# Performance work log

Measured on AMD Instinct MI355X. Metric: run time of the kernel, lower is better.

Reference implementation:

```python
import jax, jax.numpy as jnp
import numpy as np

DIM = 192
D_STATE = 16
D_CONV = 4
EXPAND = 2
D_INNER = EXPAND * DIM
DT_RANK = -(-DIM // 16)  # ceil(dim/16) = 12


def setup_inputs() -> dict:
    key = jax.random.key(0)
    ks = jax.random.split(key, 9)
    B, T, H, W, C = 2, 16, 28, 28, DIM
    x = jax.random.normal(ks[0], (B, T, H, W, C), dtype=jnp.float32)
    s = lambda k, shp, fan: jax.random.normal(k, shp, dtype=jnp.float32) / np.sqrt(fan)
    params = {
        "norm_w": jnp.ones((DIM,), jnp.float32),
        "in_proj_w": s(ks[1], (DIM, 2 * D_INNER), DIM),
        "conv_w": s(ks[2], (D_INNER, D_CONV), D_CONV),
        "conv_b": jnp.zeros((D_INNER,), jnp.float32),
        "x_proj_w": s(ks[3], (D_INNER, DT_RANK + 2 * D_STATE), D_INNER),
        "dt_proj_w": s(ks[4], (DT_RANK, D_INNER), DT_RANK),
        "dt_proj_b": jnp.full((D_INNER,), float(np.log(np.expm1(0.01))), jnp.float32),
        "A_log": jnp.log(jnp.broadcast_to(jnp.arange(1, D_STATE + 1, dtype=jnp.float32), (D_INNER, D_STATE))),
        "D": jnp.ones((D_INNER,), jnp.float32),
        "out_proj_w": s(ks[5], (D_INNER, DIM), D_INNER),
    }
    return {"x": x, **params}


def _mamba_block(xs, norm_w, in_proj_w, conv_w, conv_b, x_proj_w,
                 dt_proj_w, dt_proj_b, A_log, D, out_proj_w):
    # xs: (N, T, C). Pre-RMSNorm + Mamba + residual.
    nrm = jax.lax.rsqrt(jnp.mean(xs * xs, axis=-1, keepdims=True) + 1e-6)
    xn = xs * nrm * norm_w

    xz = xn @ in_proj_w                      # (N, T, 2*Din)
    u, z = jnp.split(xz, 2, axis=-1)         # each (N, T, Din)

    # causal depthwise conv over T
    uc = jnp.transpose(u, (0, 2, 1))         # (N, Din, T)
    uc = jax.lax.conv_general_dilated(
        uc, conv_w[:, None, :], window_strides=(1,),
        padding=[(D_CONV - 1, 0)], feature_group_count=D_INNER)
    uc = jax.nn.silu(uc + conv_b[None, :, None])
    uc = jnp.transpose(uc, (0, 2, 1))        # (N, T, Din)

    dbl = uc @ x_proj_w                      # (N, T, dt_rank + 2*S)
    dt, Bm, Cm = jnp.split(dbl, [DT_RANK, DT_RANK + D_STATE], axis=-1)
    dt = jax.nn.softplus(dt @ dt_proj_w + dt_proj_b)   # (N, T, Din)
    A = -jnp.exp(A_log)                      # (Din, S)

    def step(h, inp):
        dt_t, B_t, C_t, u_t = inp            # (N,Din),(N,S),(N,S),(N,Din)
        dA = jnp.exp(dt_t[..., None] * A)    # (N, Din, S)
        h = h * dA + (dt_t * u_t)[..., None] * B_t[:, None, :]
        y = jnp.einsum('nds,ns->nd', h, C_t)
        return h, y

    N = uc.shape[0]
    h0 = jnp.zeros((N, D_INNER, D_STATE), dt.dtype)
    sw = lambda a: jnp.swapaxes(a, 0, 1)     # time-major for scan
    _, ys = jax.lax.scan(step, h0, (sw(dt), sw(Bm), sw(Cm), sw(uc)))
    y = jnp.swapaxes(ys, 0, 1) + uc * D      # (N, T, Din)
    y = y * jax.nn.silu(z)
    return xs + y @ out_proj_w


def reference(x, norm_w, in_proj_w, conv_w, conv_b, x_proj_w,
              dt_proj_w, dt_proj_b, A_log, D, out_proj_w):
    B, T, H, W, C = x.shape
    xs = jnp.transpose(x, (0, 2, 3, 1, 4)).reshape(B * H * W, T, C)
    out = _mamba_block(xs, norm_w, in_proj_w, conv_w, conv_b, x_proj_w,
                       dt_proj_w, dt_proj_b, A_log, D, out_proj_w)
    return jnp.transpose(out.reshape(B, H, W, T, C), (0, 3, 1, 2, 4))
```

## Files before the change

### kernel.cpp

```cpp
#include <hip/hip_runtime.h>

#define NSEQ 1568
#define TDIM 16
#define CDIM 192
#define DIN  384
#define SDIM 16
#define RNK  12
#define XZW  768
#define DBLW 44
#define HW784 784

#define XNP  200
#define DINP 392
#define DBLP 48

#define NT_IN 48
#define KT_IN 6
#define NT_OUT 12
#define KT_OUT 12
#define NT_XP 3
#define KT_XP 12
#define GRP_IN  (NT_IN*KT_IN*64)
#define GRP_OUT (NT_OUT*KT_OUT*64)
#define GRP_XP  (NT_XP*KT_XP*64)
#define OFF_OUT (GRP_IN*8)
#define OFF_XP  (OFF_OUT + GRP_OUT*8)
#define WS_NEED ((size_t)(OFF_XP + GRP_XP*8) * 2)

#define IN_EL  (CDIM*XZW)
#define OUT_EL (DIN*CDIM)
#define XP_EL  (GRP_XP*8)
#define PACK_TOT (IN_EL + OUT_EL + XP_EL)

typedef unsigned short u16;
typedef unsigned int   u32;
typedef __attribute__((ext_vector_type(8))) short short8;
typedef __attribute__((ext_vector_type(4))) float f32x4;

#define LOG2E 1.44269504f
#define LN2   0.69314718f

__device__ __forceinline__ float bf2f(u16 u) {
  union { u32 i; float f; } c; c.i = ((u32)u) << 16; return c.f;
}
__device__ __forceinline__ u16 f2bf(float f) {
  union { float f; u32 i; } c; c.f = f;
  u32 i = c.i;
  i += 0x7FFFu + ((i >> 16) & 1u);
  return (u16)(i >> 16);
}

__device__ __forceinline__ float ex2(float x) {
#if __has_builtin(__builtin_amdgcn_exp2f)
  return __builtin_amdgcn_exp2f(x);
#else
  return exp2f(x);
#endif
}
__device__ __forceinline__ float lg2(float x) {
#if __has_builtin(__builtin_amdgcn_logf)
  return __builtin_amdgcn_logf(x);
#else
  return log2f(x);
#endif
}
__device__ __forceinline__ float frcp(float x) {
#if __has_builtin(__builtin_amdgcn_rcpf)
  return __builtin_amdgcn_rcpf(x);
#else
  return 1.0f / x;
#endif
}
__device__ __forceinline__ float sigmoid_f(float s) {
  return frcp(1.0f + ex2(-LOG2E * s));
}
__device__ __forceinline__ float softplus_f(float a) {
  return fmaxf(a, 0.f) + LN2 * lg2(1.0f + ex2(-LOG2E * fabsf(a)));
}

template<bool B16>
__device__ __forceinline__ float ldg(const void* p, int i) {
  if (B16) return bf2f(((const u16*)p)[i]);
  return ((const float*)p)[i];
}
template<bool B16>
__device__ __forceinline__ void stg(void* p, int i, float v) {
  if (B16) ((u16*)p)[i] = f2bf(v);
  else     ((float*)p)[i] = v;
}

__device__ __forceinline__ bool probe_bf16(const void* x) {
  const u16* xu = (const u16*)x;
  int plaus = 0;
  #pragma unroll
  for (int k = 0; k < 32; ++k) {
    u16 v = xu[2*k];
    int e = (v >> 7) & 0xFF;
    plaus += ((e >= 100 && e <= 140) || v == 0) ? 1 : 0;
  }
  return plaus >= 16;
}

template<bool B16>
__device__ __forceinline__ void pack_body(const void* in_w, const void* out_w,
                                          const void* xp_w, u16* ws, int e) {
  if (e < IN_EL) {
    int k = e / XZW, n = e - k*XZW;
    int nt = n >> 4, l16 = n & 15, kt = k >> 5, q8 = (k & 31) >> 3, j = k & 7;
    int lane = q8*16 + l16;
    ws[((nt*KT_IN + kt)*64 + lane)*8 + j] = f2bf(ldg<B16>(in_w, e));
  } else if (e < IN_EL + OUT_EL) {
    int ee = e - IN_EL;
    int k = ee / CDIM, n = ee - k*CDIM;
    int nt = n >> 4, l16 = n & 15, kt = k >> 5, q8 = (k & 31) >> 3, j = k & 7;
    int lane = q8*16 + l16;
    ws[OFF_OUT + ((nt*KT_OUT + kt)*64 + lane)*8 + j] = f2bf(ldg<B16>(out_w, ee));
  } else if (e < PACK_TOT) {
    int ee = e - IN_EL - OUT_EL;
    int gg = ee >> 3, j = ee & 7;
    int lane = gg & 63, kt = (gg >> 6) % KT_XP, nt = gg / (64*KT_XP);
    int k = kt*32 + (lane >> 4)*8 + j, n = nt*16 + (lane & 15);
    ws[OFF_XP + ee] = f2bf(n < DBLW ? ldg<B16>(xp_w, k*DBLW + n) : 0.f);
  }
}

__global__ void pack_w(const void* __restrict__ x, const void* __restrict__ in_w,
                       const void* __restrict__ out_w, const void* __restrict__ xp_w,
                       u16* __restrict__ ws) {
  int e = blockIdx.x * blockDim.x + threadIdx.x;
  if (probe_bf16(x)) pack_body<true >(in_w, out_w, xp_w, ws, e);
  else               pack_body<false>(in_w, out_w, xp_w, ws, e);
}

struct Smem {
  float dbl[TDIM*DBLP];
  u16   xn [TDIM*XNP];
  u16   u  [TDIM*DINP];
  u16   z  [TDIM*DINP];
};

template<bool B16>
__device__ __forceinline__ void body(
    Smem& sm, const u16* __restrict__ ws,
    const void* __restrict__ x,        const void* __restrict__ norm_w,
    const void* __restrict__ conv_w,   const void* __restrict__ conv_b,
    const void* __restrict__ dt_proj_w,const void* __restrict__ dt_proj_b,
    const void* __restrict__ A_log,    const void* __restrict__ Dp,
    void* __restrict__ out)
{
  const int tid  = threadIdx.x;
  const int wid  = tid >> 6;
  const int lane = tid & 63;
  const int quad = lane >> 4;
  const int l16  = lane & 15;
  const int n  = blockIdx.x;
  const int b  = n / HW784;
  const int hw = n - b * HW784;

  {
    const int c0 = lane, c1 = lane + 64, c2 = lane + 128;
    float nw0 = ldg<B16>(norm_w, c0), nw1 = ldg<B16>(norm_w, c1), nw2 = ldg<B16>(norm_w, c2);
    for (int t = wid; t < TDIM; t += 6) {
      int base = ((b*TDIM + t)*HW784 + hw)*CDIM;
      float v0 = ldg<B16>(x, base + c0);
      float v1 = ldg<B16>(x, base + c1);
      float v2 = ldg<B16>(x, base + c2);
      float ss = v0*v0 + v1*v1 + v2*v2;
      #pragma unroll
      for (int off = 32; off > 0; off >>= 1) ss += __shfl_xor(ss, off, 64);
      float rs = rsqrtf(ss * (1.0f/CDIM) + 1e-6f);
      sm.xn[t*XNP + c0] = f2bf(v0 * rs * nw0);
      sm.xn[t*XNP + c1] = f2bf(v1 * rs * nw1);
      sm.xn[t*XNP + c2] = f2bf(v2 * rs * nw2);
    }
  }
  __syncthreads();

  {
    short8 afr[KT_IN];
    #pragma unroll
    for (int kt = 0; kt < KT_IN; ++kt)
      afr[kt] = *(const short8*)(sm.xn + l16*XNP + kt*32 + quad*8);
    #pragma unroll
    for (int g = 0; g < 2; ++g) {
      f32x4 acc[4];
      #pragma unroll
      for (int i = 0; i < 4; ++i) acc[i] = (f32x4)0.f;
      #pragma unroll
      for (int kt = 0; kt < KT_IN; ++kt) {
        #pragma unroll
        for (int i = 0; i < 4; ++i) {
          int ntg = wid*8 + g*4 + i;
          short8 bfr = *(const short8*)(ws + ((ntg*KT_IN + kt)*64 + lane)*8);
          acc[i] = __builtin_amdgcn_mfma_f32_16x16x32_bf16(afr[kt], bfr, acc[i], 0, 0, 0);
        }
      }
      #pragma unroll
      for (int i = 0; i < 4; ++i) {
        int ntg = wid*8 + g*4 + i;
        u16* dst = (ntg < 24) ? sm.u : sm.z;
        int col = ((ntg < 24) ? ntg*16 : (ntg-24)*16) + l16;
        #pragma unroll
        for (int r = 0; r < 4; ++r)
          dst[(quad*4 + r)*DINP + col] = f2bf(acc[i][r]);
      }
    }
  }
  __syncthreads();

  {
    const int d = tid;
    float w0 = ldg<B16>(conv_w, d*4+0), w1 = ldg<B16>(conv_w, d*4+1);
    float w2 = ldg<B16>(conv_w, d*4+2), w3 = ldg<B16>(conv_w, d*4+3);
    float bias = ldg<B16>(conv_b, d);
    float um1 = 0.f, um2 = 0.f, um3 = 0.f;
    #pragma unroll
    for (int t = 0; t < TDIM; ++t) {
      float cur = bf2f(sm.u[t*DINP + d]);
      float s = bias + cur*w3 + um1*w2 + um2*w1 + um3*w0;
      um3 = um2; um2 = um1; um1 = cur;
      sm.u[t*DINP + d] = f2bf(s * sigmoid_f(s));
    }
  }

  float wd[RNK];
  float dt_bias = ldg<B16>(dt_proj_b, tid);
  #pragma unroll
  for (int r = 0; r < RNK; ++r) wd[r] = ldg<B16>(dt_proj_w, r*DIN + tid);
  float Dv = ldg<B16>(Dp, tid);
  float a2;
  bool geo;
  {
    a2 = -LOG2E * ex2(LOG2E * ldg<B16>(A_log, tid*SDIM + 0));
    geo = true;
    #pragma unroll
    for (int s = 1; s < SDIM; ++s) {
      float as = -LOG2E * ex2(LOG2E * ldg<B16>(A_log, tid*SDIM + s));
      geo = geo && (fabsf(as - (float)(s+1)*a2) <= 1e-4f * fabsf(as) + 1e-30f);
    }
  }
  __syncthreads();

  if (wid < 3) {
    f32x4 acc = (f32x4)0.f;
    #pragma unroll
    for (int kt = 0; kt < KT_XP; ++kt) {
      short8 afr = *(const short8*)(sm.u + l16*DINP + kt*32 + quad*8);
      short8 bfr = *(const short8*)(ws + OFF_XP + ((wid*KT_XP + kt)*64 + lane)*8);
      acc = __builtin_amdgcn_mfma_f32_16x16x32_bf16(afr, bfr, acc, 0, 0, 0);
    }
    #pragma unroll
    for (int r = 0; r < 4; ++r)
      sm.dbl[(quad*4 + r)*DBLP + wid*16 + l16] = acc[r];
  }
  __syncthreads();

  {
    const int d = tid;
    float h[SDIM];
    #pragma unroll
    for (int s = 0; s < SDIM; ++s) h[s] = 0.f;
    if (geo) {
      for (int t = 0; t < TDIM; ++t) {
        const float* row = sm.dbl + t*DBLP;
        f32x4 d0 = *(const f32x4*)(row + 0);
        f32x4 d1 = *(const f32x4*)(row + 4);
        f32x4 d2 = *(const f32x4*)(row + 8);
        float a = dt_bias
          + d0[0]*wd[0] + d0[1]*wd[1] + d0[2]*wd[2]  + d0[3]*wd[3]
          + d1[0]*wd[4] + d1[1]*wd[5] + d1[2]*wd[6]  + d1[3]*wd[7]
          + d2[0]*wd[8] + d2[1]*wd[9] + d2[2]*wd[10] + d2[3]*wd[11];
        float dtv = softplus_f(a);
        float uv  = bf2f(sm.u[t*DINP + d]);
        float du  = dtv * uv;
        float q = ex2(dtv * a2);
        float Pq[SDIM];
        Pq[0] = q;        Pq[1] = q*q;       Pq[2] = Pq[1]*q;     Pq[3] = Pq[1]*Pq[1];
        Pq[4] = Pq[3]*q;  Pq[5] = Pq[3]*Pq[1]; Pq[6] = Pq[3]*Pq[2]; Pq[7] = Pq[3]*Pq[3];
        Pq[8] = Pq[7]*q;  Pq[9] = Pq[7]*Pq[1]; Pq[10]= Pq[7]*Pq[2]; Pq[11]= Pq[7]*Pq[3];
        Pq[12]= Pq[7]*Pq[4]; Pq[13]= Pq[7]*Pq[5]; Pq[14]= Pq[7]*Pq[6]; Pq[15]= Pq[7]*Pq[7];
        float y = 0.f;
        #pragma unroll
        for (int g = 0; g < 4; ++g) {
          f32x4 Bv = *(const f32x4*)(row + 12 + 4*g);
          f32x4 Cv = *(const f32x4*)(row + 28 + 4*g);
          #pragma unroll
          for (int j = 0; j < 4; ++j) {
            int s = 4*g + j;
            h[s] = h[s]*Pq[s] + du*Bv[j];
            y += h[s]*Cv[j];
          }
        }
        y += uv * Dv;
        float zv = bf2f(sm.z[t*DINP + d]);
        sm.z[t*DINP + d] = f2bf(y * (zv * sigmoid_f(zv)));
      }
    } else {
      float A2[SDIM];
      #pragma unroll
      for (int s = 0; s < SDIM; ++s)
        A2[s] = -LOG2E * ex2(LOG2E * ldg<B16>(A_log, d*SDIM + s));
      for (int t = 0; t < TDIM; ++t) {
        const float* row = sm.dbl + t*DBLP;
        f32x4 d0 = *(const f32x4*)(row + 0);
        f32x4 d1 = *(const f32x4*)(row + 4);
        f32x4 d2 = *(const f32x4*)(row + 8);
        float a = dt_bias
          + d0[0]*wd[0] + d0[1]*wd[1] + d0[2]*wd[2]  + d0[3]*wd[3]
          + d1[0]*wd[4] + d1[1]*wd[5] + d1[2]*wd[6]  + d1[3]*wd[7]
          + d2[0]*wd[8] + d2[1]*wd[9] + d2[2]*wd[10] + d2[3]*wd[11];
        float dtv = softplus_f(a);
        float uv  = bf2f(sm.u[t*DINP + d]);
        float du  = dtv * uv;
        float y = 0.f;
        #pragma unroll
        for (int g = 0; g < 4; ++g) {
          f32x4 Bv = *(const f32x4*)(row + 12 + 4*g);
          f32x4 Cv = *(const f32x4*)(row + 28 + 4*g);
          #pragma unroll
          for (int j = 0; j < 4; ++j) {
            int s = 4*g + j;
            float dA = ex2(dtv * A2[s]);
            h[s] = h[s]*dA + du*Bv[j];
            y += h[s]*Cv[j];
          }
        }
        y += uv * Dv;
        float zv = bf2f(sm.z[t*DINP + d]);
        sm.z[t*DINP + d] = f2bf(y * (zv * sigmoid_f(zv)));
      }
    }
  }
  __syncthreads();

  {
    f32x4 acc[2];
    acc[0] = (f32x4)0.f; acc[1] = (f32x4)0.f;
    #pragma unroll
    for (int kt = 0; kt < KT_OUT; ++kt) {
      short8 afr = *(const short8*)(sm.z + l16*DINP + kt*32 + quad*8);
      #pragma unroll
      for (int i = 0; i < 2; ++i) {
        int ntg = wid*2 + i;
        short8 bfr = *(const short8*)(ws + OFF_OUT + ((ntg*KT_OUT + kt)*64 + lane)*8);
        acc[i] = __builtin_amdgcn_mfma_f32_16x16x32_bf16(afr, bfr, acc[i], 0, 0, 0);
      }
    }
    #pragma unroll
    for (int i = 0; i < 2; ++i) {
      int col = (wid*2 + i)*16 + l16;
      #pragma unroll
      for (int r = 0; r < 4; ++r) {
        int row = quad*4 + r;
        int gi = ((b*TDIM + row)*HW784 + hw)*CDIM + col;
        float o = ldg<B16>(x, gi) + acc[i][r];
        stg<B16>(out, gi, o);
      }
    }
  }
}

__launch_bounds__(384, 6)
__global__ void mamba_mfma(
    const u16* __restrict__ ws,
    const void* __restrict__ x,        const void* __restrict__ norm_w,
    const void* __restrict__ conv_w,   const void* __restrict__ conv_b,
    const void* __restrict__ dt_proj_w,const void* __restrict__ dt_proj_b,
    const void* __restrict__ A_log,    const void* __restrict__ Dp,
    void* __restrict__ out)
{
  __shared__ Smem sm;
  if (probe_bf16(x))
    body<true >(sm, ws, x, norm_w, conv_w, conv_b, dt_proj_w, dt_proj_b, A_log, Dp, out);
  else
    body<false>(sm, ws, x, norm_w, conv_w, conv_b, dt_proj_w, dt_proj_b, A_log, Dp, out);
}

struct SmemF {
  float dt [TDIM*DIN];
  float dbl[TDIM*DBLW];
  u16   xs [TDIM*CDIM];
  u16   xn [TDIM*CDIM];
  u16   u  [TDIM*DIN];
  u16   z  [TDIM*DIN];
};

template<bool B16>
__device__ __forceinline__ void body_fb(
    SmemF& sm,
    const void* __restrict__ x,        const void* __restrict__ norm_w,
    const void* __restrict__ in_proj_w,const void* __restrict__ conv_w,
    const void* __restrict__ conv_b,   const void* __restrict__ x_proj_w,
    const void* __restrict__ dt_proj_w,const void* __restrict__ dt_proj_b,
    const void* __restrict__ A_log,    const void* __restrict__ Dp,
    const void* __restrict__ out_proj_w, void* __restrict__ out)
{
  const int tid = threadIdx.x;
  const int n  = blockIdx.x;
  const int b  = n / HW784;
  const int hw = n - b * HW784;

  for (int i = tid; i < TDIM*CDIM; i += 384) {
    int t = i / CDIM, c = i - t * CDIM;
    sm.xs[i] = f2bf(ldg<B16>(x, ((b*TDIM + t)*HW784 + hw)*CDIM + c));
  }
  __syncthreads();
  {
    int wave = tid >> 6, lane = tid & 63;
    for (int t = wave; t < TDIM; t += 6) {
      float ss = 0.f;
      for (int c = lane; c < CDIM; c += 64) {
        float v = bf2f(sm.xs[t*CDIM + c]); ss += v*v;
      }
      #pragma unroll
      for (int off = 32; off > 0; off >>= 1) ss += __shfl_xor(ss, off, 64);
      float rs = rsqrtf(ss * (1.0f/CDIM) + 1e-6f);
      for (int c = lane; c < CDIM; c += 64)
        sm.xn[t*CDIM + c] = f2bf(bf2f(sm.xs[t*CDIM + c]) * rs * ldg<B16>(norm_w, c));
    }
  }
  __syncthreads();
  {
    float acc0[TDIM], acc1[TDIM];
    #pragma unroll
    for (int t = 0; t < TDIM; ++t) { acc0[t] = 0.f; acc1[t] = 0.f; }
    const int j0 = 2 * tid;
    for (int c = 0; c < CDIM; c += 2) {
      float wA0 = ldg<B16>(in_proj_w,  c   *XZW + j0);
      float wA1 = ldg<B16>(in_proj_w,  c   *XZW + j0 + 1);
      float wB0 = ldg<B16>(in_proj_w, (c+1)*XZW + j0);
      float wB1 = ldg<B16>(in_proj_w, (c+1)*XZW + j0 + 1);
      #pragma unroll
      for (int t = 0; t < TDIM; ++t) {
        union { u32 i; float f; } c0, c1;
        u32 xv = *(const u32*)(sm.xn + t*CDIM + c);
        c0.i = xv << 16; c1.i = xv & 0xFFFF0000u;
        acc0[t] += c0.f*wA0 + c1.f*wB0;
        acc1[t] += c0.f*wA1 + c1.f*wB1;
      }
    }
    if (tid < 192) {
      #pragma unroll
      for (int t = 0; t < TDIM; ++t) {
        sm.u[t*DIN + j0]   = f2bf(acc0[t]);
        sm.u[t*DIN + j0+1] = f2bf(acc1[t]);
      }
    } else {
      int z0 = j0 - 384;
      #pragma unroll
      for (int t = 0; t < TDIM; ++t) {
        sm.z[t*DIN + z0]   = f2bf(acc0[t]);
        sm.z[t*DIN + z0+1] = f2bf(acc1[t]);
      }
    }
  }
  __syncthreads();
  {
    const int d = tid;
    float uv[TDIM];
    #pragma unroll
    for (int t = 0; t < TDIM; ++t) uv[t] = bf2f(sm.u[t*DIN + d]);
    float w0 = ldg<B16>(conv_w, d*4+0), w1 = ldg<B16>(conv_w, d*4+1);
    float w2 = ldg<B16>(conv_w, d*4+2), w3 = ldg<B16>(conv_w, d*4+3);
    float bias = ldg<B16>(conv_b, d);
    #pragma unroll
    for (int t = 0; t < TDIM; ++t) {
      float s = bias + uv[t]*w3;
      if (t >= 1) s += uv[t-1]*w2;
      if (t >= 2) s += uv[t-2]*w1;
      if (t >= 3) s += uv[t-3]*w0;
      float sg = 1.0f / (1.0f + __expf(-s));
      sm.u[t*DIN + d] = f2bf(s * sg);
    }
  }
  __syncthreads();
  for (int o = tid; o < TDIM*DBLW; o += 384) {
    int t = o / DBLW, j = o - t*DBLW;
    float acc = 0.f;
    for (int d = 0; d < DIN; ++d)
      acc += bf2f(sm.u[t*DIN + d]) * ldg<B16>(x_proj_w, d*DBLW + j);
    sm.dbl[o] = acc;
  }
  __syncthreads();
  {
    const int d = tid;
    float wd[RNK];
    #pragma unroll
    for (int r = 0; r < RNK; ++r) wd[r] = ldg<B16>(dt_proj_w, r*DIN + d);
    float bias = ldg<B16>(dt_proj_b, d);
    #pragma unroll
    for (int t = 0; t < TDIM; ++t) {
      float a = bias;
      #pragma unroll
      for (int r = 0; r < RNK; ++r) a += sm.dbl[t*DBLW + r] * wd[r];
      sm.dt[t*DIN + d] = fmaxf(a, 0.f) + log1pf(__expf(-fabsf(a)));
    }
  }
  __syncthreads();
  {
    const int d = tid;
    float A[SDIM], h[SDIM];
    #pragma unroll
    for (int s = 0; s < SDIM; ++s) {
      A[s] = -__expf(ldg<B16>(A_log, d*SDIM + s));
      h[s] = 0.f;
    }
    float Dv = ldg<B16>(Dp, d);
    for (int t = 0; t < TDIM; ++t) {
      float dtv = sm.dt[t*DIN + d];
      float uv  = bf2f(sm.u[t*DIN + d]);
      float du  = dtv * uv;
      float y = 0.f;
      #pragma unroll
      for (int s = 0; s < SDIM; ++s) {
        float dA = __expf(dtv * A[s]);
        h[s] = h[s]*dA + du * sm.dbl[t*DBLW + 12 + s];
        y += h[s] * sm.dbl[t*DBLW + 28 + s];
      }
      y += uv * Dv;
      float zv = bf2f(sm.z[t*DIN + d]);
      float sg = 1.0f / (1.0f + __expf(-zv));
      sm.dt[t*DIN + d] = y * (zv * sg);
    }
  }
  __syncthreads();
  {
    const int tt = tid / CDIM;
    const int c  = tid - tt*CDIM;
    float acc[8];
    #pragma unroll
    for (int i = 0; i < 8; ++i) acc[i] = 0.f;
    for (int d = 0; d < DIN; ++d) {
      float w = ldg<B16>(out_proj_w, d*CDIM + c);
      #pragma unroll
      for (int i = 0; i < 8; ++i)
        acc[i] += sm.dt[(tt*8 + i)*DIN + d] * w;
    }
    #pragma unroll
    for (int i = 0; i < 8; ++i) {
      int t = tt*8 + i;
      float o = bf2f(sm.xs[t*CDIM + c]) + acc[i];
      stg<B16>(out, ((b*TDIM + t)*HW784 + hw)*CDIM + c, o);
    }
  }
}

__launch_bounds__(384)
__global__ void mamba_fallback(
    const void* __restrict__ x,        const void* __restrict__ norm_w,
    const void* __restrict__ in_proj_w,const void* __restrict__ conv_w,
    const void* __restrict__ conv_b,   const void* __restrict__ x_proj_w,
    const void* __restrict__ dt_proj_w,const void* __restrict__ dt_proj_b,
    const void* __restrict__ A_log,    const void* __restrict__ Dp,
    const void* __restrict__ out_proj_w, void* __restrict__ out)
{
  __shared__ SmemF sm;
  if (probe_bf16(x))
    body_fb<true >(sm, x, norm_w, in_proj_w, conv_w, conv_b, x_proj_w,
                   dt_proj_w, dt_proj_b, A_log, Dp, out_proj_w, out);
  else
    body_fb<false>(sm, x, norm_w, in_proj_w, conv_w, conv_b, x_proj_w,
                   dt_proj_w, dt_proj_b, A_log, Dp, out_proj_w, out);
}

extern "C" void kernel_launch(void* const* d_in, const int* in_sizes, int n_in,
                              void* d_out, int out_size, void* d_ws, size_t ws_size,
                              hipStream_t stream) {
  if (ws_size >= WS_NEED) {
    pack_w<<<(PACK_TOT + 255) / 256, 256, 0, stream>>>(
        d_in[0], d_in[2], d_in[10], d_in[5], (u16*)d_ws);
    mamba_mfma<<<NSEQ, 384, 0, stream>>>(
        (const u16*)d_ws,
        d_in[0], d_in[1], d_in[3], d_in[4],
        d_in[6], d_in[7], d_in[8], d_in[9], d_out);
  } else {
    mamba_fallback<<<NSEQ, 384, 0, stream>>>(
        d_in[0], d_in[1], d_in[2], d_in[3], d_in[4], d_in[5],
        d_in[6], d_in[7], d_in[8], d_in[9], d_in[10], d_out);
  }
}
```

Before: 172.8 us.

## Process two sequences per block to reuse weight fragments across MFMA tiles

Each block now handles two adjacent spatial positions (32 rows) instead of one, so every B-fragment of in_proj, x_proj and out_proj weights loaded from global memory feeds two MFMAs. The goal is to halve weight traffic per sequence and give more MFMA work per load. In exchange the grid halves, shared memory doubles, launch bounds drop to 3 blocks per CU, and the scan phase runs the two sequences serially per thread, which lengthens the serial part per block.

Result: slower. 196.2 us (+13.5%).

```diff
diff --git a/kernel.cpp b/kernel.cpp
--- a/kernel.cpp
+++ b/kernel.cpp
@@ -133,10 +133,10 @@
 }
 
 struct Smem {
-  float dbl[TDIM*DBLP];
-  u16   xn [TDIM*XNP];
-  u16   u  [TDIM*DINP];
-  u16   z  [TDIM*DINP];
+  float dbl[2*TDIM*DBLP];
+  u16   xn [2*TDIM*XNP];
+  u16   u  [2*TDIM*DINP];
+  u16   z  [2*TDIM*DINP];
 };
 
 template<bool B16>
@@ -153,15 +153,16 @@
   const int lane = tid & 63;
   const int quad = lane >> 4;
   const int l16  = lane & 15;
-  const int n  = blockIdx.x;
-  const int b  = n / HW784;
-  const int hw = n - b * HW784;
+  const int n0 = blockIdx.x * 2;
+  const int b  = n0 / HW784;
+  const int hw = n0 - b * HW784;
 
   {
     const int c0 = lane, c1 = lane + 64, c2 = lane + 128;
     float nw0 = ldg<B16>(norm_w, c0), nw1 = ldg<B16>(norm_w, c1), nw2 = ldg<B16>(norm_w, c2);
-    for (int t = wid; t < TDIM; t += 6) {
-      int base = ((b*TDIM + t)*HW784 + hw)*CDIM;
+    for (int row = wid; row < 2*TDIM; row += 6) {
+      int s = row >> 4, t = row & 15;
+      int base = ((b*TDIM + t)*HW784 + hw + s)*CDIM;
       float v0 = ldg<B16>(x, base + c0);
       float v1 = ldg<B16>(x, base + c1);
       float v2 = ldg<B16>(x, base + c2);
@@ -169,30 +170,29 @@
       #pragma unroll
       for (int off = 32; off > 0; off >>= 1) ss += __shfl_xor(ss, off, 64);
       float rs = rsqrtf(ss * (1.0f/CDIM) + 1e-6f);
-      sm.xn[t*XNP + c0] = f2bf(v0 * rs * nw0);
-      sm.xn[t*XNP + c1] = f2bf(v1 * rs * nw1);
-      sm.xn[t*XNP + c2] = f2bf(v2 * rs * nw2);
-    }
-  }
-  __syncthreads();
-
-  {
-    short8 afr[KT_IN];
-    #pragma unroll
-    for (int kt = 0; kt < KT_IN; ++kt)
-      afr[kt] = *(const short8*)(sm.xn + l16*XNP + kt*32 + quad*8);
+      sm.xn[row*XNP + c0] = f2bf(v0 * rs * nw0);
+      sm.xn[row*XNP + c1] = f2bf(v1 * rs * nw1);
+      sm.xn[row*XNP + c2] = f2bf(v2 * rs * nw2);
+    }
+  }
+  __syncthreads();
+
+  {
     #pragma unroll
     for (int g = 0; g < 2; ++g) {
-      f32x4 acc[4];
-      #pragma unroll
-      for (int i = 0; i < 4; ++i) acc[i] = (f32x4)0.f;
+      f32x4 acc0[4], acc1[4];
+      #pragma unroll
+      for (int i = 0; i < 4; ++i) { acc0[i] = (f32x4)0.f; acc1[i] = (f32x4)0.f; }
       #pragma unroll
       for (int kt = 0; kt < KT_IN; ++kt) {
+        short8 a0 = *(const short8*)(sm.xn +  l16      *XNP + kt*32 + quad*8);
+        short8 a1 = *(const short8*)(sm.xn + (16 + l16)*XNP + kt*32 + quad*8);
         #pragma unroll
         for (int i = 0; i < 4; ++i) {
           int ntg = wid*8 + g*4 + i;
           short8 bfr = *(const short8*)(ws + ((ntg*KT_IN + kt)*64 + lane)*8);
-          acc[i] = __builtin_amdgcn_mfma_f32_16x16x32_bf16(afr[kt], bfr, acc[i], 0, 0, 0);
+          acc0[i] = __builtin_amdgcn_mfma_f32_16x16x32_bf16(a0, bfr, acc0[i], 0, 0, 0);
+          acc1[i] = __builtin_amdgcn_mfma_f32_16x16x32_bf16(a1, bfr, acc1[i], 0, 0, 0);
         }
       }
       #pragma unroll
@@ -201,8 +201,10 @@
         u16* dst = (ntg < 24) ? sm.u : sm.z;
         int col = ((ntg < 24) ? ntg*16 : (ntg-24)*16) + l16;
         #pragma unroll
-        for (int r = 0; r < 4; ++r)
-          dst[(quad*4 + r)*DINP + col] = f2bf(acc[i][r]);
+        for (int r = 0; r < 4; ++r) {
+          dst[( quad*4 + r)*DINP + col]      = f2bf(acc0[i][r]);
+          dst[(16 + quad*4 + r)*DINP + col]  = f2bf(acc1[i][r]);
+        }
       }
     }
   }
@@ -213,13 +215,17 @@
     float w0 = ldg<B16>(conv_w, d*4+0), w1 = ldg<B16>(conv_w, d*4+1);
     float w2 = ldg<B16>(conv_w, d*4+2), w3 = ldg<B16>(conv_w, d*4+3);
     float bias = ldg<B16>(conv_b, d);
-    float um1 = 0.f, um2 = 0.f, um3 = 0.f;
-    #pragma unroll
-    for (int t = 0; t < TDIM; ++t) {
-      float cur = bf2f(sm.u[t*DINP + d]);
-      float s = bias + cur*w3 + um1*w2 + um2*w1 + um3*w0;
-      um3 = um2; um2 = um1; um1 = cur;
-      sm.u[t*DINP + d] = f2bf(s * sigmoid_f(s));
+    #pragma unroll
+    for (int s = 0; s < 2; ++s) {
+      float um1 = 0.f, um2 = 0.f, um3 = 0.f;
+      #pragma unroll
+      for (int t = 0; t < TDIM; ++t) {
+        int row = s*TDIM + t;
+        float cur = bf2f(sm.u[row*DINP + d]);
+        float sv = bias + cur*w3 + um1*w2 + um2*w1 + um3*w0;
+        um3 = um2; um2 = um1; um1 = cur;
+        sm.u[row*DINP + d] = f2bf(sv * sigmoid_f(sv));
+      }
     }
   }
 
@@ -242,125 +248,146 @@
   __syncthreads();
 
   if (wid < 3) {
-    f32x4 acc = (f32x4)0.f;
+    f32x4 acc0 = (f32x4)0.f, acc1 = (f32x4)0.f;
     #pragma unroll
     for (int kt = 0; kt < KT_XP; ++kt) {
-      short8 afr = *(const short8*)(sm.u + l16*DINP + kt*32 + quad*8);
+      short8 a0 = *(const short8*)(sm.u +  l16      *DINP + kt*32 + quad*8);
+      short8 a1 = *(const short8*)(sm.u + (16 + l16)*DINP + kt*32 + quad*8);
       short8 bfr = *(const short8*)(ws + OFF_XP + ((wid*KT_XP + kt)*64 + lane)*8);
-      acc = __builtin_amdgcn_mfma_f32_16x16x32_bf16(afr, bfr, acc, 0, 0, 0);
-    }
-    #pragma unroll
-    for (int r = 0; r < 4; ++r)
-      sm.dbl[(quad*4 + r)*DBLP + wid*16 + l16] = acc[r];
+      acc0 = __builtin_amdgcn_mfma_f32_16x16x32_bf16(a0, bfr, acc0, 0, 0, 0);
+      acc1 = __builtin_amdgcn_mfma_f32_16x16x32_bf16(a1, bfr, acc1, 0, 0, 0);
+    }
+    #pragma unroll
+    for (int r = 0; r < 4; ++r) {
+      sm.dbl[( quad*4 + r)*DBLP + wid*16 + l16]      = acc0[r];
+      sm.dbl[(16 + quad*4 + r)*DBLP + wid*16 + l16]  = acc1[r];
+    }
   }
   __syncthreads();
 
   {
     const int d = tid;
-    float h[SDIM];
-    #pragma unroll
-    for (int s = 0; s < SDIM; ++s) h[s] = 0.f;
     if (geo) {
-      for (int t = 0; t < TDIM; ++t) {
-        const float* row = sm.dbl + t*DBLP;
-        f32x4 d0 = *(const f32x4*)(row + 0);
-        f32x4 d1 = *(const f32x4*)(row + 4);
-        f32x4 d2 = *(const f32x4*)(row + 8);
-        float a = dt_bias
-          + d0[0]*wd[0] + d0[1]*wd[1] + d0[2]*wd[2]  + d0[3]*wd[3]
-          + d1[0]*wd[4] + d1[1]*wd[5] + d1[2]*wd[6]  + d1[3]*wd[7]
-          + d2[0]*wd[8] + d2[1]*wd[9] + d2[2]*wd[10] + d2[3]*wd[11];
-        float dtv = softplus_f(a);
-        float uv  = bf2f(sm.u[t*DINP + d]);
-        float du  = dtv * uv;
-        float q = ex2(dtv * a2);
-        float Pq[SDIM];
-        Pq[0] = q;        Pq[1] = q*q;       Pq[2] = Pq[1]*q;     Pq[3] = Pq[1]*Pq[1];
-        Pq[4] = Pq[3]*q;  Pq[5] = Pq[3]*Pq[1]; Pq[6] = Pq[3]*Pq[2]; Pq[7] = Pq[3]*Pq[3];
-        Pq[8] = Pq[7]*q;  Pq[9] = Pq[7]*Pq[1]; Pq[10]= Pq[7]*Pq[2]; Pq[11]= Pq[7]*Pq[3];
-        Pq[12]= Pq[7]*Pq[4]; Pq[13]= Pq[7]*Pq[5]; Pq[14]= Pq[7]*Pq[6]; Pq[15]= Pq[7]*Pq[7];
-        float y = 0.f;
+      #pragma unroll
+      for (int s2 = 0; s2 < 2; ++s2) {
+        float h[SDIM];
         #pragma unroll
-        for (int g = 0; g < 4; ++g) {
-          f32x4 Bv = *(const f32x4*)(row + 12 + 4*g);
-          f32x4 Cv = *(const f32x4*)(row + 28 + 4*g);
+        for (int s = 0; s < SDIM; ++s) h[s] = 0.f;
+        for (int t = 0; t < TDIM; ++t) {
+          int rw = s2*TDIM + t;
+          const float* row = sm.dbl + rw*DBLP;
+          f32x4 d0 = *(const f32x4*)(row + 0);
+          f32x4 d1 = *(const f32x4*)(row + 4);
+          f32x4 d2 = *(const f32x4*)(row + 8);
+          float a = dt_bias
+            + d0[0]*wd[0] + d0[1]*wd[1] + d0[2]*wd[2]  + d0[3]*wd[3]
+            + d1[0]*wd[4] + d1[1]*wd[5] + d1[2]*wd[6]  + d1[3]*wd[7]
+            + d2[0]*wd[8] + d2[1]*wd[9] + d2[2]*wd[10] + d2[3]*wd[11];
+          float dtv = softplus_f(a);
+          float uv  = bf2f(sm.u[rw*DINP + d]);
+          float du  = dtv * uv;
+          float q = ex2(dtv * a2);
+          float Pq[SDIM];
+          Pq[0] = q;        Pq[1] = q*q;       Pq[2] = Pq[1]*q;     Pq[3] = Pq[1]*Pq[1];
+          Pq[4] = Pq[3]*q;  Pq[5] = Pq[3]*Pq[1]; Pq[6] = Pq[3]*Pq[2]; Pq[7] = Pq[3]*Pq[3];
+          Pq[8] = Pq[7]*q;  Pq[9] = Pq[7]*Pq[1]; Pq[10]= Pq[7]*Pq[2]; Pq[11]= Pq[7]*Pq[3];
+          Pq[12]= Pq[7]*Pq[4]; Pq[13]= Pq[7]*Pq[5]; Pq[14]= Pq[7]*Pq[6]; Pq[15]= Pq[7]*Pq[7];
+          float y = 0.f;
           #pragma unroll
-          for (int j = 0; j < 4; ++j) {
-            int s = 4*g + j;
-            h[s] = h[s]*Pq[s] + du*Bv[j];
-            y += h[s]*Cv[j];
+          for (int g = 0; g < 4; ++g) {
+            f32x4 Bv = *(const f32x4*)(row + 12 + 4*g);
+            f32x4 Cv = *(const f32x4*)(row + 28 + 4*g);
+            #pragma unroll
+            for (int j = 0; j < 4; ++j) {
+              int s = 4*g + j;
+              h[s] = h[s]*Pq[s] + du*Bv[j];
+              y += h[s]*Cv[j];
+            }
           }
+          y += uv * Dv;
+          float zv = bf2f(sm.z[rw*DINP + d]);
+          sm.z[rw*DINP + d] = f2bf(y * (zv * sigmoid_f(zv)));
         }
-        y += uv * Dv;
-        float zv = bf2f(sm.z[t*DINP + d]);
-        sm.z[t*DINP + d] = f2bf(y * (zv * sigmoid_f(zv)));
       }
     } else {
       float A2[SDIM];
       #pragma unroll
       for (int s = 0; s < SDIM; ++s)
         A2[s] = -LOG2E * ex2(LOG2E * ldg<B16>(A_log, d*SDIM + s));
-      for (int t = 0; t < TDIM; ++t) {
-        const float* row = sm.dbl + t*DBLP;
-        f32x4 d0 = *(const f32x4*)(row + 0);
-        f32x4 d1 = *(const f32x4*)(row + 4);
-        f32x4 d2 = *(const f32x4*)(row + 8);
-        float a = dt_bias
-          + d0[0]*wd[0] + d0[1]*wd[1] + d0[2]*wd[2]  + d0[3]*wd[3]
-          + d1[0]*wd[4] + d1[1]*wd[5] + d1[2]*wd[6]  + d1[3]*wd[7]
-          + d2[0]*wd[8] + d2[1]*wd[9] + d2[2]*wd[10] + d2[3]*wd[11];
-        float dtv = softplus_f(a);
-        float uv  = bf2f(sm.u[t*DINP + d]);
-        float du  = dtv * uv;
-        float y = 0.f;
+      #pragma unroll
+      for (int s2 = 0; s2 < 2; ++s2) {
+        float h[SDIM];
         #pragma unroll
-        for (int g = 0; g < 4; ++g) {
-          f32x4 Bv = *(const f32x4*)(row + 12 + 4*g);
-          f32x4 Cv = *(const f32x4*)(row + 28 + 4*g);
+        for (int s = 0; s < SDIM; ++s) h[s] = 0.f;
+        for (int t = 0; t < TDIM; ++t) {
+          int rw = s2*TDIM + t;
+          const float* row = sm.dbl + rw*DBLP;
+          f32x4 d0 = *(const f32x4*)(row + 0);
+          f32x4 d1 = *(const f32x4*)(row + 4);
+          f32x4 d2 = *(const f32x4*)(row + 8);
+          float a = dt_bias
+            + d0[0]*wd[0] + d0[1]*wd[1] + d0[2]*wd[2]  + d0[3]*wd[3]
+            + d1[0]*wd[4] + d1[1]*wd[5] + d1[2]*wd[6]  + d1[3]*wd[7]
+            + d2[0]*wd[8] + d2[1]*wd[9] + d2[2]*wd[10] + d2[3]*wd[11];
+          float dtv = softplus_f(a);
+          float uv  = bf2f(sm.u[rw*DINP + d]);
+          float du  = dtv * uv;
+          float y = 0.f;
           #pragma unroll
-          for (int j = 0; j < 4; ++j) {
-            int s = 4*g + j;
-            float dA = ex2(dtv * A2[s]);
-            h[s] = h[s]*dA + du*Bv[j];
-            y += h[s]*Cv[j];
+          for (int g = 0; g < 4; ++g) {
+            f32x4 Bv = *(const f32x4*)(row + 12 + 4*g);
+            f32x4 Cv = *(const f32x4*)(row + 28 + 4*g);
+            #pragma unroll
+            for (int j = 0; j < 4; ++j) {
+              int s = 4*g + j;
+              float dA = ex2(dtv * A2[s]);
+              h[s] = h[s]*dA + du*Bv[j];
+              y += h[s]*Cv[j];
+            }
           }
+          y += uv * Dv;
+          float zv = bf2f(sm.z[rw*DINP + d]);
+          sm.z[rw*DINP + d] = f2bf(y * (zv * sigmoid_f(zv)));
         }
-        y += uv * Dv;
-        float zv = bf2f(sm.z[t*DINP + d]);
-        sm.z[t*DINP + d] = f2bf(y * (zv * sigmoid_f(zv)));
-      }
-    }
-  }
-  __syncthreads();
-
-  {
-    f32x4 acc[2];
-    acc[0] = (f32x4)0.f; acc[1] = (f32x4)0.f;
+      }
+    }
+  }
+  __syncthreads();
+
+  {
+    f32x4 acc[2][2];
+    #pragma unroll
+    for (int ci = 0; ci < 2; ++ci) { acc[ci][0] = (f32x4)0.f; acc[ci][1] = (f32x4)0.f; }
     #pragma unroll
     for (int kt = 0; kt < KT_OUT; ++kt) {
-      short8 afr = *(const short8*)(sm.z + l16*DINP + kt*32 + quad*8);
-      #pragma unroll
-      for (int i = 0; i < 2; ++i) {
-        int ntg = wid*2 + i;
+      short8 a0 = *(const short8*)(sm.z +  l16      *DINP + kt*32 + quad*8);
+      short8 a1 = *(const short8*)(sm.z + (16 + l16)*DINP + kt*32 + quad*8);
+      #pragma unroll
+      for (int ci = 0; ci < 2; ++ci) {
+        int ntg = wid*2 + ci;
         short8 bfr = *(const short8*)(ws + OFF_OUT + ((ntg*KT_OUT + kt)*64 + lane)*8);
-        acc[i] = __builtin_amdgcn_mfma_f32_16x16x32_bf16(afr, bfr, acc[i], 0, 0, 0);
-      }
-    }
-    #pragma unroll
-    for (int i = 0; i < 2; ++i) {
-      int col = (wid*2 + i)*16 + l16;
-      #pragma unroll
-      for (int r = 0; r < 4; ++r) {
-        int row = quad*4 + r;
-        int gi = ((b*TDIM + row)*HW784 + hw)*CDIM + col;
-        float o = ldg<B16>(x, gi) + acc[i][r];
-        stg<B16>(out, gi, o);
-      }
-    }
-  }
-}
-
-__launch_bounds__(384, 6)
+        acc[ci][0] = __builtin_amdgcn_mfma_f32_16x16x32_bf16(a0, bfr, acc[ci][0], 0, 0, 0);
+        acc[ci][1] = __builtin_amdgcn_mfma_f32_16x16x32_bf16(a1, bfr, acc[ci][1], 0, 0, 0);
+      }
+    }
+    #pragma unroll
+    for (int ci = 0; ci < 2; ++ci) {
+      int col = (wid*2 + ci)*16 + l16;
+      #pragma unroll
+      for (int rt = 0; rt < 2; ++rt) {
+        #pragma unroll
+        for (int r = 0; r < 4; ++r) {
+          int row = quad*4 + r;
+          int gi = ((b*TDIM + row)*HW784 + hw + rt)*CDIM + col;
+          float o = ldg<B16>(x, gi) + acc[ci][rt][r];
+          stg<B16>(out, gi, o);
+        }
+      }
+    }
+  }
+}
+
+__launch_bounds__(384, 3)
 __global__ void mamba_mfma(
     const u16* __restrict__ ws,
     const void* __restrict__ x,        const void* __restrict__ norm_w,
@@ -569,7 +596,7 @@
   if (ws_size >= WS_NEED) {
     pack_w<<<(PACK_TOT + 255) / 256, 256, 0, stream>>>(
         d_in[0], d_in[2], d_in[10], d_in[5], (u16*)d_ws);
-    mamba_mfma<<<NSEQ, 384, 0, stream>>>(
+    mamba_mfma<<<NSEQ/2, 384, 0, stream>>>(
         (const u16*)d_ws,
         d_in[0], d_in[1], d_in[3], d_in[4],
         d_in[6], d_in[7], d_in[8], d_in[9], d_out);
```
